# Kernel optimization log

Hardware: AMD Instinct MI355X
Metric: run time of the kernel (lower is better)

Reference implementation:

```python
import jax, jax.numpy as jnp
import numpy as np

V, E, H = 32000, 50, 100
B, T = 8, 512


def setup_inputs() -> dict:
    key = jax.random.key(0)
    ks = jax.random.split(key, 12)
    inputs = jax.random.randint(ks[0], (B, T), 0, V, dtype=jnp.int64)
    d = {
        "inputs": inputs,
        "embedding": jax.random.normal(ks[1], (V, E), jnp.float32),
        "W_hr": jax.random.normal(ks[2], (H, H), jnp.float32) * 0.01,
        "W_xr": jax.random.normal(ks[3], (E, H), jnp.float32) * 0.01,
        "b_r": jnp.zeros((H,), jnp.float32),
        "W_hz": jax.random.normal(ks[4], (H, H), jnp.float32) * 0.01,
        "W_xz": jax.random.normal(ks[5], (E, H), jnp.float32) * 0.01,
        "b_z": jnp.zeros((H,), jnp.float32),
        "W_hh": jax.random.normal(ks[6], (H, H), jnp.float32) * 0.01,
        "W_xh": jax.random.normal(ks[7], (E, H), jnp.float32) * 0.01,
        "b_h": jnp.zeros((H,), jnp.float32),
        "fc_W": jax.random.normal(ks[8], (H, V), jnp.float32) * 0.01,
        "fc_b": jnp.zeros((V,), jnp.float32),
    }
    return d


def reference(inputs, embedding, W_hr, W_xr, b_r, W_hz, W_xz, b_z,
              W_hh, W_xh, b_h, fc_W, fc_b):
    # Embed all timesteps at once: [B, T, E] -> time-major [T, B, E]
    x = embedding[inputs]
    x_tm = jnp.transpose(x, (1, 0, 2))

    h0 = jnp.zeros((inputs.shape[0], W_hr.shape[0]), dtype=embedding.dtype)

    def step(h_t, x_t):
        R_t = jax.nn.sigmoid(h_t @ W_hr + x_t @ W_xr + b_r)
        Z_t = jax.nn.sigmoid(h_t @ W_hz + x_t @ W_xz + b_z)
        # NOTE: original torch code computes (R_t * h_t) @ W_hh (left-to-right precedence)
        h_tilda = jnp.tanh((R_t * h_t) @ W_hh + x_t @ W_xh + b_h)
        h_new = Z_t * h_tilda + (1.0 - Z_t) * h_t
        y_t = h_new @ fc_W + fc_b  # [B, V]
        return h_new, y_t

    _, ys = jax.lax.scan(step, h0, x_tm)  # ys: [T, B, V]
    return jnp.transpose(ys, (1, 0, 2))   # [B, T, V]
```

## Files before the change

kernel.cpp:

```cpp
#include <hip/hip_runtime.h>
#include <hip/hip_bf16.h>
#include <hip/hip_fp16.h>
#include <math.h>

#define NV 32000
#define NE 50
#define NH 100
#define NB 8
#define NT 512
#define KP 112
#define HS 136

typedef __attribute__((ext_vector_type(8)))  _Float16 f16x8;
typedef __attribute__((ext_vector_type(4)))  float    f32x4;
typedef __attribute__((ext_vector_type(16))) float    f32x16;

__device__ __forceinline__ void bar_lgkm() {
    __builtin_amdgcn_sched_barrier(0);
    asm volatile("s_waitcnt lgkmcnt(0)" ::: "memory");
    __builtin_amdgcn_s_barrier();
    asm volatile("" ::: "memory");
    __builtin_amdgcn_sched_barrier(0);
}

__global__ __launch_bounds__(256) void convw_kernel(
    const float* __restrict__ W, _Float16* __restrict__ Wp)
{
    int wv = threadIdx.x >> 6, l = threadIdx.x & 63;
    int ct = blockIdx.x * 4 + wv;
    int v  = ct * 32 + (l & 31);
    int kb = (l >> 5) * 8;
    _Float16* dst = Wp + (size_t)ct * 7 * 512 + l * 8;
    for (int kt = 0; kt < 7; kt++) {
        f16x8 tmp;
        #pragma unroll
        for (int j = 0; j < 8; j++) {
            int k = kt * 16 + kb + j;
            tmp[j] = (_Float16)(k < NH ? W[(size_t)k * NV + v] : 0.0f);
        }
        *(f16x8*)(dst + (size_t)kt * 512) = tmp;
    }
}

__global__ __launch_bounds__(64) void convg_kernel(
    const float* __restrict__ Whr, const float* __restrict__ Whz,
    const float* __restrict__ Whh, _Float16* __restrict__ Wg)
{
    int f = blockIdx.x;
    int g = f / 28, rem = f % 28, n = rem / 4, kt = rem % 4;
    const float* W = (g == 0) ? Whr : (g == 1) ? Whz : Whh;
    int l   = threadIdx.x;
    int col = n * 16 + (l & 15);
    int k0  = kt * 32 + (l >> 4) * 8;
    f16x8 v;
    #pragma unroll
    for (int j = 0; j < 8; j++) {
        int k = k0 + j;
        v[j] = (_Float16)((k < NH && col < NH) ? W[k * NH + col] : 0.0f);
    }
    *(f16x8*)(Wg + (size_t)f * 512 + l * 8) = v;
}

__global__ __launch_bounds__(128) void xproj_kernel(
    const int* __restrict__ inp, const float* __restrict__ emb,
    const float* __restrict__ Wxr, const float* __restrict__ br,
    const float* __restrict__ Wxz, const float* __restrict__ bz,
    const float* __restrict__ Wxh, const float* __restrict__ bh,
    float* __restrict__ Xr, float* __restrict__ Xz, float* __restrict__ Xh)
{
    int n = blockIdx.x;
    int t = n >> 3, b = n & 7;
    __shared__ float xs[NE];
    int tid = threadIdx.x;
    int idx = inp[b * NT + t];
    if (tid < NE) xs[tid] = emb[idx * NE + tid];
    __syncthreads();
    if (tid < NH) {
        float ar = br[tid], az = bz[tid], ah = bh[tid];
        for (int e = 0; e < NE; e++) {
            float x = xs[e];
            ar += x * Wxr[e * NH + tid];
            az += x * Wxz[e * NH + tid];
            ah += x * Wxh[e * NH + tid];
        }
        Xr[n * NH + tid] = ar;
        Xz[n * NH + tid] = az;
        Xh[n * NH + tid] = ah;
    }
}

__global__ __launch_bounds__(256) void gru_rec_kernel(
    const _Float16* __restrict__ Wg,
    const float* __restrict__ Xr, const float* __restrict__ Xz,
    const float* __restrict__ Xh, _Float16* __restrict__ Hp)
{
    int b   = blockIdx.x;
    int tid = threadIdx.x;
    int w   = tid >> 6, l = tid & 63;
    int lj  = l & 15;

    __shared__ __align__(16) _Float16 h16[16 * HS];
    __shared__ __align__(16) _Float16 rh16[16 * HS];
    for (int i = tid; i < 16 * HS; i += 256) { h16[i] = (_Float16)0.0f; rh16[i] = (_Float16)0.0f; }
    __syncthreads();

    int n0 = w, n1 = w + 4;
    bool has1 = (n1 < 7);
    int n1c = has1 ? n1 : n0;

    f16x8 WR0[4], WZ0[4], WH0[4], WR1[4], WZ1[4], WH1[4];
    #pragma unroll
    for (int kt = 0; kt < 4; kt++) {
        WR0[kt] = *(const f16x8*)(Wg + (size_t)(((0*7 + n0)*4 + kt))*512 + l*8);
        WZ0[kt] = *(const f16x8*)(Wg + (size_t)(((1*7 + n0)*4 + kt))*512 + l*8);
        WH0[kt] = *(const f16x8*)(Wg + (size_t)(((2*7 + n0)*4 + kt))*512 + l*8);
        WR1[kt] = *(const f16x8*)(Wg + (size_t)(((0*7 + n1c)*4 + kt))*512 + l*8);
        WZ1[kt] = *(const f16x8*)(Wg + (size_t)(((1*7 + n1c)*4 + kt))*512 + l*8);
        WH1[kt] = *(const f16x8*)(Wg + (size_t)(((2*7 + n1c)*4 + kt))*512 + l*8);
    }

    int j0 = n0 * 16 + lj;
    int j1 = n1c * 16 + lj;
    int j0x = j0 < NH ? j0 : NH - 1;
    int j1x = j1 < NH ? j1 : NH - 1;

    float h0 = 0.0f, h1 = 0.0f;
    float xr0, xz0, xh0, xr1, xz1, xh1;
    if (l < 16) {
        int base = b * NH;
        xr0 = Xr[base + j0x]; xz0 = Xz[base + j0x]; xh0 = Xh[base + j0x];
        xr1 = Xr[base + j1x]; xz1 = Xz[base + j1x]; xh1 = Xh[base + j1x];
    }

    int aoff = lj * HS + (l >> 4) * 8;

    for (int t = 0; t < NT; t++) {
        float pr0, pz0, ph0, pr1, pz1, ph1;
        if (l < 16 && t + 1 < NT) {
            int base = ((t + 1) * NB + b) * NH;
            pr0 = Xr[base + j0x]; pz0 = Xz[base + j0x]; ph0 = Xh[base + j0x];
            pr1 = Xr[base + j1x]; pz1 = Xz[base + j1x]; ph1 = Xh[base + j1x];
        }

        f32x4 aR0 = {0,0,0,0}, aZ0 = {0,0,0,0}, aR1 = {0,0,0,0}, aZ1 = {0,0,0,0};
        #pragma unroll
        for (int kt = 0; kt < 4; kt++) {
            f16x8 a = *(const f16x8*)&h16[aoff + kt * 32];
            aR0 = __builtin_amdgcn_mfma_f32_16x16x32_f16(a, WR0[kt], aR0, 0, 0, 0);
            aZ0 = __builtin_amdgcn_mfma_f32_16x16x32_f16(a, WZ0[kt], aZ0, 0, 0, 0);
            aR1 = __builtin_amdgcn_mfma_f32_16x16x32_f16(a, WR1[kt], aR1, 0, 0, 0);
            aZ1 = __builtin_amdgcn_mfma_f32_16x16x32_f16(a, WZ1[kt], aZ1, 0, 0, 0);
        }
        float z0 = 0.0f, z1 = 0.0f;
        if (l < 16) {
            float r0 = 1.0f / (1.0f + __expf(-(aR0[0] + xr0)));
            z0       = 1.0f / (1.0f + __expf(-(aZ0[0] + xz0)));
            rh16[j0] = (_Float16)(j0 < NH ? r0 * h0 : 0.0f);
            if (has1) {
                float r1 = 1.0f / (1.0f + __expf(-(aR1[0] + xr1)));
                z1       = 1.0f / (1.0f + __expf(-(aZ1[0] + xz1)));
                rh16[j1] = (_Float16)(j1 < NH ? r1 * h1 : 0.0f);
            }
        }
        bar_lgkm();

        f32x4 aH0 = {0,0,0,0}, aH1 = {0,0,0,0};
        #pragma unroll
        for (int kt = 0; kt < 4; kt++) {
            f16x8 a = *(const f16x8*)&rh16[aoff + kt * 32];
            aH0 = __builtin_amdgcn_mfma_f32_16x16x32_f16(a, WH0[kt], aH0, 0, 0, 0);
            aH1 = __builtin_amdgcn_mfma_f32_16x16x32_f16(a, WH1[kt], aH1, 0, 0, 0);
        }
        if (l < 16) {
            size_t hpb = (size_t)(t * NB + b) * KP;
            {
                float e  = __expf(2.0f * (aH0[0] + xh0));
                float ht = 1.0f - 2.0f / (e + 1.0f);
                float hn = fmaf(z0, ht - h0, h0);
                hn = (j0 < NH) ? hn : 0.0f;
                h0 = hn;
                h16[j0] = (_Float16)hn;
                Hp[hpb + j0] = (_Float16)hn;
            }
            if (has1) {
                float e  = __expf(2.0f * (aH1[0] + xh1));
                float ht = 1.0f - 2.0f / (e + 1.0f);
                float hn = fmaf(z1, ht - h1, h1);
                hn = (j1 < NH) ? hn : 0.0f;
                h1 = hn;
                h16[j1] = (_Float16)hn;
                Hp[hpb + j1] = (_Float16)hn;
            }
        }
        bar_lgkm();

        xr0 = pr0; xz0 = pz0; xh0 = ph0;
        xr1 = pr1; xz1 = pz1; xh1 = ph1;
    }
}

__global__ __launch_bounds__(256) void outgemm_kernel(
    const _Float16* __restrict__ Hp, const _Float16* __restrict__ Wp,
    const float* __restrict__ fcb, float* __restrict__ out)
{
    int tid = threadIdx.x;
    int wv = tid >> 6, l = tid & 63;
    int n0 = blockIdx.x * 32;
    int cb = blockIdx.y * 256 + wv * 64;

    const _Float16* arow = Hp + (size_t)(n0 + (l & 31)) * KP + (l >> 5) * 8;
    f16x8 a[7];
    #pragma unroll
    for (int kt = 0; kt < 7; kt++)
        a[kt] = *(const f16x8*)(arow + kt * 16);

    int ct0 = cb >> 5;
    const _Float16* bp = Wp + (size_t)ct0 * 7 * 512 + l * 8;

    f32x16 acc0 = {0,0,0,0,0,0,0,0,0,0,0,0,0,0,0,0};
    f32x16 acc1 = {0,0,0,0,0,0,0,0,0,0,0,0,0,0,0,0};
    #pragma unroll
    for (int kt = 0; kt < 7; kt++) {
        f16x8 b0 = *(const f16x8*)(bp + (size_t)kt * 512);
        f16x8 b1 = *(const f16x8*)(bp + (size_t)(kt + 7) * 512);
        acc0 = __builtin_amdgcn_mfma_f32_32x32x16_f16(a[kt], b0, acc0, 0, 0, 0);
        acc1 = __builtin_amdgcn_mfma_f32_32x32x16_f16(a[kt], b1, acc1, 0, 0, 0);
    }

    int c0 = cb + (l & 31);
    float bias0 = fcb[c0], bias1 = fcb[c0 + 32];
    #pragma unroll
    for (int p = 0; p < 16; p++) {
        int r = (p & 3) + 8 * (p >> 2) + 4 * (l >> 5);
        int m = n0 + r;
        size_t row = (size_t)(m & 7) * NT + (m >> 3);
        out[row * NV + c0]      = acc0[p] + bias0;
        out[row * NV + c0 + 32] = acc1[p] + bias1;
    }
}

extern "C" void kernel_launch(void* const* d_in, const int* in_sizes, int n_in,
                              void* d_out, int out_size, void* d_ws, size_t ws_size,
                              hipStream_t stream)
{
    const int*   inp = (const int*)  d_in[0];
    const float* emb = (const float*)d_in[1];
    const float* Whr = (const float*)d_in[2];
    const float* Wxr = (const float*)d_in[3];
    const float* br  = (const float*)d_in[4];
    const float* Whz = (const float*)d_in[5];
    const float* Wxz = (const float*)d_in[6];
    const float* bz  = (const float*)d_in[7];
    const float* Whh = (const float*)d_in[8];
    const float* Wxh = (const float*)d_in[9];
    const float* bh  = (const float*)d_in[10];
    const float* fcW = (const float*)d_in[11];
    const float* fcb = (const float*)d_in[12];
    float* out = (float*)d_out;

    float*    Xr = (float*)d_ws;
    float*    Xz = Xr + NT * NB * NH;
    float*    Xh = Xz + NT * NB * NH;
    _Float16* Hp = (_Float16*)(Xh + NT * NB * NH);
    _Float16* Wp = Hp + (size_t)NT * NB * KP;
    _Float16* Wg = Wp + (size_t)1000 * 7 * 512;

    convw_kernel<<<NV / 32 / 4, 256, 0, stream>>>(fcW, Wp);
    convg_kernel<<<84, 64, 0, stream>>>(Whr, Whz, Whh, Wg);
    xproj_kernel<<<NT * NB, 128, 0, stream>>>(inp, emb, Wxr, br, Wxz, bz, Wxh, bh,
                                              Xr, Xz, Xh);
    gru_rec_kernel<<<NB, 256, 0, stream>>>(Wg, Xr, Xz, Xh, Hp);
    dim3 ggrid(NT * NB / 32, NV / 256);
    outgemm_kernel<<<ggrid, 256, 0, stream>>>(Hp, Wp, fcb, out);
}
```

Baseline: 636.8 us.

## Fuse GRU recurrence and output GEMM into a persistent producer-consumer kernel

```diff
diff --git a/kernel.cpp b/kernel.cpp
--- a/kernel.cpp
+++ b/kernel.cpp
@@ -11,6 +11,12 @@
 #define KP 112
 #define HS 136
 
+#define NBLK   256
+#define NCONS  (NBLK - NB)
+#define NMT    (NT * NB / 32)
+#define NNT    (NV / 256)
+#define NTILE  (NMT * NNT)
+
 typedef __attribute__((ext_vector_type(8)))  _Float16 f16x8;
 typedef __attribute__((ext_vector_type(4)))  float    f32x4;
 typedef __attribute__((ext_vector_type(16))) float    f32x16;
@@ -21,6 +27,11 @@
     __builtin_amdgcn_s_barrier();
     asm volatile("" ::: "memory");
     __builtin_amdgcn_sched_barrier(0);
+}
+
+__global__ void init_kernel(int* __restrict__ ctr)
+{
+    if (threadIdx.x < NB) ctr[threadIdx.x] = 0;
 }
 
 __global__ __launch_bounds__(256) void convw_kernel(
@@ -89,153 +100,183 @@
     }
 }
 
-__global__ __launch_bounds__(256) void gru_rec_kernel(
+__global__ __launch_bounds__(256) void fused_kernel(
     const _Float16* __restrict__ Wg,
     const float* __restrict__ Xr, const float* __restrict__ Xz,
-    const float* __restrict__ Xh, _Float16* __restrict__ Hp)
-{
-    int b   = blockIdx.x;
-    int tid = threadIdx.x;
-    int w   = tid >> 6, l = tid & 63;
-    int lj  = l & 15;
-
+    const float* __restrict__ Xh, _Float16* __restrict__ Hp,
+    const _Float16* __restrict__ Wp, const float* __restrict__ fcb,
+    float* __restrict__ out, int* __restrict__ ctr)
+{
     __shared__ __align__(16) _Float16 h16[16 * HS];
     __shared__ __align__(16) _Float16 rh16[16 * HS];
-    for (int i = tid; i < 16 * HS; i += 256) { h16[i] = (_Float16)0.0f; rh16[i] = (_Float16)0.0f; }
-    __syncthreads();
-
-    int n0 = w, n1 = w + 4;
-    bool has1 = (n1 < 7);
-    int n1c = has1 ? n1 : n0;
-
-    f16x8 WR0[4], WZ0[4], WH0[4], WR1[4], WZ1[4], WH1[4];
-    #pragma unroll
-    for (int kt = 0; kt < 4; kt++) {
-        WR0[kt] = *(const f16x8*)(Wg + (size_t)(((0*7 + n0)*4 + kt))*512 + l*8);
-        WZ0[kt] = *(const f16x8*)(Wg + (size_t)(((1*7 + n0)*4 + kt))*512 + l*8);
-        WH0[kt] = *(const f16x8*)(Wg + (size_t)(((2*7 + n0)*4 + kt))*512 + l*8);
-        WR1[kt] = *(const f16x8*)(Wg + (size_t)(((0*7 + n1c)*4 + kt))*512 + l*8);
-        WZ1[kt] = *(const f16x8*)(Wg + (size_t)(((1*7 + n1c)*4 + kt))*512 + l*8);
-        WH1[kt] = *(const f16x8*)(Wg + (size_t)(((2*7 + n1c)*4 + kt))*512 + l*8);
-    }
-
-    int j0 = n0 * 16 + lj;
-    int j1 = n1c * 16 + lj;
-    int j0x = j0 < NH ? j0 : NH - 1;
-    int j1x = j1 < NH ? j1 : NH - 1;
-
-    float h0 = 0.0f, h1 = 0.0f;
-    float xr0, xz0, xh0, xr1, xz1, xh1;
-    if (l < 16) {
-        int base = b * NH;
-        xr0 = Xr[base + j0x]; xz0 = Xz[base + j0x]; xh0 = Xh[base + j0x];
-        xr1 = Xr[base + j1x]; xz1 = Xz[base + j1x]; xh1 = Xh[base + j1x];
-    }
-
-    int aoff = lj * HS + (l >> 4) * 8;
-
-    for (int t = 0; t < NT; t++) {
-        float pr0, pz0, ph0, pr1, pz1, ph1;
-        if (l < 16 && t + 1 < NT) {
-            int base = ((t + 1) * NB + b) * NH;
-            pr0 = Xr[base + j0x]; pz0 = Xz[base + j0x]; ph0 = Xh[base + j0x];
-            pr1 = Xr[base + j1x]; pz1 = Xz[base + j1x]; ph1 = Xh[base + j1x];
-        }
-
-        f32x4 aR0 = {0,0,0,0}, aZ0 = {0,0,0,0}, aR1 = {0,0,0,0}, aZ1 = {0,0,0,0};
+
+    int tid = threadIdx.x;
+
+    if (blockIdx.x < NB) {
+        __builtin_amdgcn_s_setprio(1);
+        int b   = blockIdx.x;
+        int w   = tid >> 6, l = tid & 63;
+        int lj  = l & 15;
+
+        for (int i = tid; i < 16 * HS; i += 256) { h16[i] = (_Float16)0.0f; rh16[i] = (_Float16)0.0f; }
+        __syncthreads();
+
+        int n0 = w, n1 = w + 4;
+        bool has1 = (n1 < 7);
+        int n1c = has1 ? n1 : n0;
+
+        f16x8 WR0[4], WZ0[4], WH0[4], WR1[4], WZ1[4], WH1[4];
         #pragma unroll
         for (int kt = 0; kt < 4; kt++) {
-            f16x8 a = *(const f16x8*)&h16[aoff + kt * 32];
-            aR0 = __builtin_amdgcn_mfma_f32_16x16x32_f16(a, WR0[kt], aR0, 0, 0, 0);
-            aZ0 = __builtin_amdgcn_mfma_f32_16x16x32_f16(a, WZ0[kt], aZ0, 0, 0, 0);
-            aR1 = __builtin_amdgcn_mfma_f32_16x16x32_f16(a, WR1[kt], aR1, 0, 0, 0);
-            aZ1 = __builtin_amdgcn_mfma_f32_16x16x32_f16(a, WZ1[kt], aZ1, 0, 0, 0);
-        }
-        float z0 = 0.0f, z1 = 0.0f;
+            WR0[kt] = *(const f16x8*)(Wg + (size_t)(((0*7 + n0)*4 + kt))*512 + l*8);
+            WZ0[kt] = *(const f16x8*)(Wg + (size_t)(((1*7 + n0)*4 + kt))*512 + l*8);
+            WH0[kt] = *(const f16x8*)(Wg + (size_t)(((2*7 + n0)*4 + kt))*512 + l*8);
+            WR1[kt] = *(const f16x8*)(Wg + (size_t)(((0*7 + n1c)*4 + kt))*512 + l*8);
+            WZ1[kt] = *(const f16x8*)(Wg + (size_t)(((1*7 + n1c)*4 + kt))*512 + l*8);
+            WH1[kt] = *(const f16x8*)(Wg + (size_t)(((2*7 + n1c)*4 + kt))*512 + l*8);
+        }
+
+        int j0 = n0 * 16 + lj;
+        int j1 = n1c * 16 + lj;
+        int j0x = j0 < NH ? j0 : NH - 1;
+        int j1x = j1 < NH ? j1 : NH - 1;
+
+        float h0 = 0.0f, h1 = 0.0f;
+        float xr0, xz0, xh0, xr1, xz1, xh1;
         if (l < 16) {
-            float r0 = 1.0f / (1.0f + __expf(-(aR0[0] + xr0)));
-            z0       = 1.0f / (1.0f + __expf(-(aZ0[0] + xz0)));
-            rh16[j0] = (_Float16)(j0 < NH ? r0 * h0 : 0.0f);
-            if (has1) {
-                float r1 = 1.0f / (1.0f + __expf(-(aR1[0] + xr1)));
-                z1       = 1.0f / (1.0f + __expf(-(aZ1[0] + xz1)));
-                rh16[j1] = (_Float16)(j1 < NH ? r1 * h1 : 0.0f);
-            }
-        }
-        bar_lgkm();
-
-        f32x4 aH0 = {0,0,0,0}, aH1 = {0,0,0,0};
-        #pragma unroll
-        for (int kt = 0; kt < 4; kt++) {
-            f16x8 a = *(const f16x8*)&rh16[aoff + kt * 32];
-            aH0 = __builtin_amdgcn_mfma_f32_16x16x32_f16(a, WH0[kt], aH0, 0, 0, 0);
-            aH1 = __builtin_amdgcn_mfma_f32_16x16x32_f16(a, WH1[kt], aH1, 0, 0, 0);
-        }
-        if (l < 16) {
-            size_t hpb = (size_t)(t * NB + b) * KP;
-            {
-                float e  = __expf(2.0f * (aH0[0] + xh0));
-                float ht = 1.0f - 2.0f / (e + 1.0f);
-                float hn = fmaf(z0, ht - h0, h0);
-                hn = (j0 < NH) ? hn : 0.0f;
-                h0 = hn;
-                h16[j0] = (_Float16)hn;
-                Hp[hpb + j0] = (_Float16)hn;
-            }
-            if (has1) {
-                float e  = __expf(2.0f * (aH1[0] + xh1));
-                float ht = 1.0f - 2.0f / (e + 1.0f);
-                float hn = fmaf(z1, ht - h1, h1);
-                hn = (j1 < NH) ? hn : 0.0f;
-                h1 = hn;
-                h16[j1] = (_Float16)hn;
-                Hp[hpb + j1] = (_Float16)hn;
-            }
-        }
-        bar_lgkm();
-
-        xr0 = pr0; xz0 = pz0; xh0 = ph0;
-        xr1 = pr1; xz1 = pz1; xh1 = ph1;
-    }
-}
-
-__global__ __launch_bounds__(256) void outgemm_kernel(
-    const _Float16* __restrict__ Hp, const _Float16* __restrict__ Wp,
-    const float* __restrict__ fcb, float* __restrict__ out)
-{
-    int tid = threadIdx.x;
-    int wv = tid >> 6, l = tid & 63;
-    int n0 = blockIdx.x * 32;
-    int cb = blockIdx.y * 256 + wv * 64;
-
-    const _Float16* arow = Hp + (size_t)(n0 + (l & 31)) * KP + (l >> 5) * 8;
-    f16x8 a[7];
-    #pragma unroll
-    for (int kt = 0; kt < 7; kt++)
-        a[kt] = *(const f16x8*)(arow + kt * 16);
-
-    int ct0 = cb >> 5;
-    const _Float16* bp = Wp + (size_t)ct0 * 7 * 512 + l * 8;
-
-    f32x16 acc0 = {0,0,0,0,0,0,0,0,0,0,0,0,0,0,0,0};
-    f32x16 acc1 = {0,0,0,0,0,0,0,0,0,0,0,0,0,0,0,0};
-    #pragma unroll
-    for (int kt = 0; kt < 7; kt++) {
-        f16x8 b0 = *(const f16x8*)(bp + (size_t)kt * 512);
-        f16x8 b1 = *(const f16x8*)(bp + (size_t)(kt + 7) * 512);
-        acc0 = __builtin_amdgcn_mfma_f32_32x32x16_f16(a[kt], b0, acc0, 0, 0, 0);
-        acc1 = __builtin_amdgcn_mfma_f32_32x32x16_f16(a[kt], b1, acc1, 0, 0, 0);
-    }
-
-    int c0 = cb + (l & 31);
-    float bias0 = fcb[c0], bias1 = fcb[c0 + 32];
-    #pragma unroll
-    for (int p = 0; p < 16; p++) {
-        int r = (p & 3) + 8 * (p >> 2) + 4 * (l >> 5);
-        int m = n0 + r;
-        size_t row = (size_t)(m & 7) * NT + (m >> 3);
-        out[row * NV + c0]      = acc0[p] + bias0;
-        out[row * NV + c0 + 32] = acc1[p] + bias1;
+            int base = b * NH;
+            xr0 = Xr[base + j0x]; xz0 = Xz[base + j0x]; xh0 = Xh[base + j0x];
+            xr1 = Xr[base + j1x]; xz1 = Xz[base + j1x]; xh1 = Xh[base + j1x];
+        }
+
+        int aoff = lj * HS + (l >> 4) * 8;
+
+        for (int t = 0; t < NT; t++) {
+            float pr0, pz0, ph0, pr1, pz1, ph1;
+            if (l < 16 && t + 1 < NT) {
+                int base = ((t + 1) * NB + b) * NH;
+                pr0 = Xr[base + j0x]; pz0 = Xz[base + j0x]; ph0 = Xh[base + j0x];
+                pr1 = Xr[base + j1x]; pz1 = Xz[base + j1x]; ph1 = Xh[base + j1x];
+            }
+
+            f32x4 aR0 = {0,0,0,0}, aZ0 = {0,0,0,0}, aR1 = {0,0,0,0}, aZ1 = {0,0,0,0};
+            #pragma unroll
+            for (int kt = 0; kt < 4; kt++) {
+                f16x8 a = *(const f16x8*)&h16[aoff + kt * 32];
+                aR0 = __builtin_amdgcn_mfma_f32_16x16x32_f16(a, WR0[kt], aR0, 0, 0, 0);
+                aZ0 = __builtin_amdgcn_mfma_f32_16x16x32_f16(a, WZ0[kt], aZ0, 0, 0, 0);
+                aR1 = __builtin_amdgcn_mfma_f32_16x16x32_f16(a, WR1[kt], aR1, 0, 0, 0);
+                aZ1 = __builtin_amdgcn_mfma_f32_16x16x32_f16(a, WZ1[kt], aZ1, 0, 0, 0);
+            }
+            float z0 = 0.0f, z1 = 0.0f;
+            if (l < 16) {
+                float r0 = 1.0f / (1.0f + __expf(-(aR0[0] + xr0)));
+                z0       = 1.0f / (1.0f + __expf(-(aZ0[0] + xz0)));
+                rh16[j0] = (_Float16)(j0 < NH ? r0 * h0 : 0.0f);
+                if (has1) {
+                    float r1 = 1.0f / (1.0f + __expf(-(aR1[0] + xr1)));
+                    z1       = 1.0f / (1.0f + __expf(-(aZ1[0] + xz1)));
+                    rh16[j1] = (_Float16)(j1 < NH ? r1 * h1 : 0.0f);
+                }
+            }
+            bar_lgkm();
+
+            f32x4 aH0 = {0,0,0,0}, aH1 = {0,0,0,0};
+            #pragma unroll
+            for (int kt = 0; kt < 4; kt++) {
+                f16x8 a = *(const f16x8*)&rh16[aoff + kt * 32];
+                aH0 = __builtin_amdgcn_mfma_f32_16x16x32_f16(a, WH0[kt], aH0, 0, 0, 0);
+                aH1 = __builtin_amdgcn_mfma_f32_16x16x32_f16(a, WH1[kt], aH1, 0, 0, 0);
+            }
+            if (l < 16) {
+                size_t hpb = (size_t)(t * NB + b) * KP;
+                {
+                    float e  = __expf(2.0f * (aH0[0] + xh0));
+                    float ht = 1.0f - 2.0f / (e + 1.0f);
+                    float hn = fmaf(z0, ht - h0, h0);
+                    hn = (j0 < NH) ? hn : 0.0f;
+                    h0 = hn;
+                    h16[j0] = (_Float16)hn;
+                    Hp[hpb + j0] = (_Float16)hn;
+                }
+                if (has1) {
+                    float e  = __expf(2.0f * (aH1[0] + xh1));
+                    float ht = 1.0f - 2.0f / (e + 1.0f);
+                    float hn = fmaf(z1, ht - h1, h1);
+                    hn = (j1 < NH) ? hn : 0.0f;
+                    h1 = hn;
+                    h16[j1] = (_Float16)hn;
+                    Hp[hpb + j1] = (_Float16)hn;
+                }
+            }
+            bar_lgkm();
+
+            if ((t & 7) == 7) {
+                asm volatile("s_waitcnt vmcnt(0)" ::: "memory");
+                __syncthreads();
+                if (tid == 0)
+                    __hip_atomic_store(ctr + b, t + 1, __ATOMIC_RELEASE,
+                                       __HIP_MEMORY_SCOPE_AGENT);
+            }
+
+            xr0 = pr0; xz0 = pz0; xh0 = ph0;
+            xr1 = pr1; xz1 = pz1; xh1 = ph1;
+        }
+    } else {
+        int wv = tid >> 6, l = tid & 63;
+        int done_upto = 0;
+
+        for (int tile = (int)blockIdx.x - NB; tile < NTILE; tile += NCONS) {
+            int mt  = tile / NNT;
+            int ntl = tile - mt * NNT;
+            int need = mt * 4 + 4;
+
+            if (need > done_upto) {
+                if (tid == 0) {
+                    #pragma unroll 1
+                    for (int bi = 0; bi < NB; ++bi)
+                        while (__hip_atomic_load(ctr + bi, __ATOMIC_RELAXED,
+                                                 __HIP_MEMORY_SCOPE_AGENT) < need)
+                            __builtin_amdgcn_s_sleep(8);
+                }
+                __syncthreads();
+                __builtin_amdgcn_fence(__ATOMIC_ACQUIRE, "agent");
+                done_upto = need;
+            }
+
+            int n0 = mt * 32;
+            int cb = ntl * 256 + wv * 64;
+
+            const _Float16* arow = Hp + (size_t)(n0 + (l & 31)) * KP + (l >> 5) * 8;
+            f16x8 a[7];
+            #pragma unroll
+            for (int kt = 0; kt < 7; kt++)
+                a[kt] = *(const f16x8*)(arow + kt * 16);
+
+            int ct0 = cb >> 5;
+            const _Float16* bp = Wp + (size_t)ct0 * 7 * 512 + l * 8;
+
+            f32x16 acc0 = {0,0,0,0,0,0,0,0,0,0,0,0,0,0,0,0};
+            f32x16 acc1 = {0,0,0,0,0,0,0,0,0,0,0,0,0,0,0,0};
+            #pragma unroll
+            for (int kt = 0; kt < 7; kt++) {
+                f16x8 b0 = *(const f16x8*)(bp + (size_t)kt * 512);
+                f16x8 b1 = *(const f16x8*)(bp + (size_t)(kt + 7) * 512);
+                acc0 = __builtin_amdgcn_mfma_f32_32x32x16_f16(a[kt], b0, acc0, 0, 0, 0);
+                acc1 = __builtin_amdgcn_mfma_f32_32x32x16_f16(a[kt], b1, acc1, 0, 0, 0);
+            }
+
+            int c0 = cb + (l & 31);
+            float bias0 = fcb[c0], bias1 = fcb[c0 + 32];
+            #pragma unroll
+            for (int p = 0; p < 16; p++) {
+                int r = (p & 3) + 8 * (p >> 2) + 4 * (l >> 5);
+                int m = n0 + r;
+                size_t row = (size_t)(m & 7) * NT + (m >> 3);
+                out[row * NV + c0]      = acc0[p] + bias0;
+                out[row * NV + c0 + 32] = acc1[p] + bias1;
+            }
+        }
     }
 }
 
@@ -264,12 +305,12 @@
     _Float16* Hp = (_Float16*)(Xh + NT * NB * NH);
     _Float16* Wp = Hp + (size_t)NT * NB * KP;
     _Float16* Wg = Wp + (size_t)1000 * 7 * 512;
-
+    int*      ct = (int*)(Wg + (size_t)84 * 512);
+
+    init_kernel<<<1, 64, 0, stream>>>(ct);
     convw_kernel<<<NV / 32 / 4, 256, 0, stream>>>(fcW, Wp);
     convg_kernel<<<84, 64, 0, stream>>>(Whr, Whz, Whh, Wg);
     xproj_kernel<<<NT * NB, 128, 0, stream>>>(inp, emb, Wxr, br, Wxz, bz, Wxh, bh,
                                               Xr, Xz, Xh);
-    gru_rec_kernel<<<NB, 256, 0, stream>>>(Wg, Xr, Xz, Xh, Hp);
-    dim3 ggrid(NT * NB / 32, NV / 256);
-    outgemm_kernel<<<ggrid, 256, 0, stream>>>(Hp, Wp, fcb, out);
-}
+    fused_kernel<<<NBLK, 256, 0, stream>>>(Wg, Xr, Xz, Xh, Hp, Wp, fcb, out, ct);
+}
```

Measured after the change: 962.9 us. +51.2%, slower.

## Run GRU recurrence in a single wavefront per batch with register-resident weights

Applied to the files above, without the earlier changes.

```diff
diff --git a/kernel.cpp b/kernel.cpp
--- a/kernel.cpp
+++ b/kernel.cpp
@@ -9,19 +9,10 @@
 #define NB 8
 #define NT 512
 #define KP 112
-#define HS 136
 
 typedef __attribute__((ext_vector_type(8)))  _Float16 f16x8;
 typedef __attribute__((ext_vector_type(4)))  float    f32x4;
 typedef __attribute__((ext_vector_type(16))) float    f32x16;
-
-__device__ __forceinline__ void bar_lgkm() {
-    __builtin_amdgcn_sched_barrier(0);
-    asm volatile("s_waitcnt lgkmcnt(0)" ::: "memory");
-    __builtin_amdgcn_s_barrier();
-    asm volatile("" ::: "memory");
-    __builtin_amdgcn_sched_barrier(0);
-}
 
 __global__ __launch_bounds__(256) void convw_kernel(
     const float* __restrict__ W, _Float16* __restrict__ Wp)
@@ -89,113 +80,118 @@
     }
 }
 
-__global__ __launch_bounds__(256) void gru_rec_kernel(
+__global__ __launch_bounds__(64, 1) void gru_rec_kernel(
     const _Float16* __restrict__ Wg,
     const float* __restrict__ Xr, const float* __restrict__ Xz,
     const float* __restrict__ Xh, _Float16* __restrict__ Hp)
 {
-    int b   = blockIdx.x;
-    int tid = threadIdx.x;
-    int w   = tid >> 6, l = tid & 63;
-    int lj  = l & 15;
-
-    __shared__ __align__(16) _Float16 h16[16 * HS];
-    __shared__ __align__(16) _Float16 rh16[16 * HS];
-    for (int i = tid; i < 16 * HS; i += 256) { h16[i] = (_Float16)0.0f; rh16[i] = (_Float16)0.0f; }
+    const int b  = blockIdx.x;
+    const int l  = threadIdx.x;
+    const int kg = l >> 4;
+
+    __shared__ __align__(16) _Float16 h16[128];
+    __shared__ __align__(16) _Float16 rh16[128];
+    h16[l]  = (_Float16)0.0f;  h16[l + 64]  = (_Float16)0.0f;
+    rh16[l] = (_Float16)0.0f;  rh16[l + 64] = (_Float16)0.0f;
     __syncthreads();
 
-    int n0 = w, n1 = w + 4;
-    bool has1 = (n1 < 7);
-    int n1c = has1 ? n1 : n0;
-
-    f16x8 WR0[4], WZ0[4], WH0[4], WR1[4], WZ1[4], WH1[4];
-    #pragma unroll
-    for (int kt = 0; kt < 4; kt++) {
-        WR0[kt] = *(const f16x8*)(Wg + (size_t)(((0*7 + n0)*4 + kt))*512 + l*8);
-        WZ0[kt] = *(const f16x8*)(Wg + (size_t)(((1*7 + n0)*4 + kt))*512 + l*8);
-        WH0[kt] = *(const f16x8*)(Wg + (size_t)(((2*7 + n0)*4 + kt))*512 + l*8);
-        WR1[kt] = *(const f16x8*)(Wg + (size_t)(((0*7 + n1c)*4 + kt))*512 + l*8);
-        WZ1[kt] = *(const f16x8*)(Wg + (size_t)(((1*7 + n1c)*4 + kt))*512 + l*8);
-        WH1[kt] = *(const f16x8*)(Wg + (size_t)(((2*7 + n1c)*4 + kt))*512 + l*8);
-    }
-
-    int j0 = n0 * 16 + lj;
-    int j1 = n1c * 16 + lj;
-    int j0x = j0 < NH ? j0 : NH - 1;
-    int j1x = j1 < NH ? j1 : NH - 1;
-
-    float h0 = 0.0f, h1 = 0.0f;
-    float xr0, xz0, xh0, xr1, xz1, xh1;
+    f16x8 WB[3][7][4];
+    #pragma unroll
+    for (int g = 0; g < 3; g++)
+        #pragma unroll
+        for (int n = 0; n < 7; n++)
+            #pragma unroll
+            for (int kt = 0; kt < 4; kt++)
+                WB[g][n][kt] = *(const f16x8*)(Wg + (size_t)((g*7 + n)*4 + kt)*512 + l*8);
+
+    float hcol[7], zv[7], xcr[7], xcz[7], xch[7];
+    int   cx[7];
+    #pragma unroll
+    for (int n = 0; n < 7; n++) {
+        hcol[n] = 0.f; zv[n] = 0.f; xcr[n] = 0.f; xcz[n] = 0.f; xch[n] = 0.f;
+        int c = n * 16 + l;
+        cx[n] = c < NH ? c : NH - 1;
+    }
+
     if (l < 16) {
         int base = b * NH;
-        xr0 = Xr[base + j0x]; xz0 = Xz[base + j0x]; xh0 = Xh[base + j0x];
-        xr1 = Xr[base + j1x]; xz1 = Xz[base + j1x]; xh1 = Xh[base + j1x];
-    }
-
-    int aoff = lj * HS + (l >> 4) * 8;
+        #pragma unroll
+        for (int n = 0; n < 7; n++) {
+            xcr[n] = Xr[base + cx[n]];
+            xcz[n] = Xz[base + cx[n]];
+            xch[n] = Xh[base + cx[n]];
+        }
+    }
 
     for (int t = 0; t < NT; t++) {
-        float pr0, pz0, ph0, pr1, pz1, ph1;
+        f16x8 Ah[4];
+        #pragma unroll
+        for (int kt = 0; kt < 4; kt++)
+            Ah[kt] = *(const f16x8*)&h16[kg * 8 + kt * 32];
+
+        f32x4 aR[7], aZ[7];
+        #pragma unroll
+        for (int n = 0; n < 7; n++) {
+            aR[n] = (f32x4){xcr[n], 0.f, 0.f, 0.f};
+            aZ[n] = (f32x4){xcz[n], 0.f, 0.f, 0.f};
+        }
         if (l < 16 && t + 1 < NT) {
             int base = ((t + 1) * NB + b) * NH;
-            pr0 = Xr[base + j0x]; pz0 = Xz[base + j0x]; ph0 = Xh[base + j0x];
-            pr1 = Xr[base + j1x]; pz1 = Xz[base + j1x]; ph1 = Xh[base + j1x];
-        }
-
-        f32x4 aR0 = {0,0,0,0}, aZ0 = {0,0,0,0}, aR1 = {0,0,0,0}, aZ1 = {0,0,0,0};
+            #pragma unroll
+            for (int n = 0; n < 7; n++) {
+                xcr[n] = Xr[base + cx[n]];
+                xcz[n] = Xz[base + cx[n]];
+            }
+        }
         #pragma unroll
         for (int kt = 0; kt < 4; kt++) {
-            f16x8 a = *(const f16x8*)&h16[aoff + kt * 32];
-            aR0 = __builtin_amdgcn_mfma_f32_16x16x32_f16(a, WR0[kt], aR0, 0, 0, 0);
-            aZ0 = __builtin_amdgcn_mfma_f32_16x16x32_f16(a, WZ0[kt], aZ0, 0, 0, 0);
-            aR1 = __builtin_amdgcn_mfma_f32_16x16x32_f16(a, WR1[kt], aR1, 0, 0, 0);
-            aZ1 = __builtin_amdgcn_mfma_f32_16x16x32_f16(a, WZ1[kt], aZ1, 0, 0, 0);
-        }
-        float z0 = 0.0f, z1 = 0.0f;
+            #pragma unroll
+            for (int n = 0; n < 7; n++) {
+                aR[n] = __builtin_amdgcn_mfma_f32_16x16x32_f16(Ah[kt], WB[0][n][kt], aR[n], 0, 0, 0);
+                aZ[n] = __builtin_amdgcn_mfma_f32_16x16x32_f16(Ah[kt], WB[1][n][kt], aZ[n], 0, 0, 0);
+            }
+        }
         if (l < 16) {
-            float r0 = 1.0f / (1.0f + __expf(-(aR0[0] + xr0)));
-            z0       = 1.0f / (1.0f + __expf(-(aZ0[0] + xz0)));
-            rh16[j0] = (_Float16)(j0 < NH ? r0 * h0 : 0.0f);
-            if (has1) {
-                float r1 = 1.0f / (1.0f + __expf(-(aR1[0] + xr1)));
-                z1       = 1.0f / (1.0f + __expf(-(aZ1[0] + xz1)));
-                rh16[j1] = (_Float16)(j1 < NH ? r1 * h1 : 0.0f);
-            }
-        }
-        bar_lgkm();
-
-        f32x4 aH0 = {0,0,0,0}, aH1 = {0,0,0,0};
-        #pragma unroll
-        for (int kt = 0; kt < 4; kt++) {
-            f16x8 a = *(const f16x8*)&rh16[aoff + kt * 32];
-            aH0 = __builtin_amdgcn_mfma_f32_16x16x32_f16(a, WH0[kt], aH0, 0, 0, 0);
-            aH1 = __builtin_amdgcn_mfma_f32_16x16x32_f16(a, WH1[kt], aH1, 0, 0, 0);
-        }
+            #pragma unroll
+            for (int n = 0; n < 7; n++) {
+                float r = 1.0f / (1.0f + __expf(-aR[n][0]));
+                zv[n]   = 1.0f / (1.0f + __expf(-aZ[n][0]));
+                rh16[n * 16 + l] = (_Float16)(r * hcol[n]);
+            }
+        }
+
+        f16x8 Ar[4];
+        #pragma unroll
+        for (int kt = 0; kt < 4; kt++)
+            Ar[kt] = *(const f16x8*)&rh16[kg * 8 + kt * 32];
+
+        f32x4 aH[7];
+        #pragma unroll
+        for (int n = 0; n < 7; n++) aH[n] = (f32x4){xch[n], 0.f, 0.f, 0.f};
+        if (l < 16 && t + 1 < NT) {
+            int base = ((t + 1) * NB + b) * NH;
+            #pragma unroll
+            for (int n = 0; n < 7; n++) xch[n] = Xh[base + cx[n]];
+        }
+        #pragma unroll
+        for (int kt = 0; kt < 4; kt++)
+            #pragma unroll
+            for (int n = 0; n < 7; n++)
+                aH[n] = __builtin_amdgcn_mfma_f32_16x16x32_f16(Ar[kt], WB[2][n][kt], aH[n], 0, 0, 0);
+
         if (l < 16) {
-            size_t hpb = (size_t)(t * NB + b) * KP;
-            {
-                float e  = __expf(2.0f * (aH0[0] + xh0));
-                float ht = 1.0f - 2.0f / (e + 1.0f);
-                float hn = fmaf(z0, ht - h0, h0);
-                hn = (j0 < NH) ? hn : 0.0f;
-                h0 = hn;
-                h16[j0] = (_Float16)hn;
-                Hp[hpb + j0] = (_Float16)hn;
-            }
-            if (has1) {
-                float e  = __expf(2.0f * (aH1[0] + xh1));
-                float ht = 1.0f - 2.0f / (e + 1.0f);
-                float hn = fmaf(z1, ht - h1, h1);
-                hn = (j1 < NH) ? hn : 0.0f;
-                h1 = hn;
-                h16[j1] = (_Float16)hn;
-                Hp[hpb + j1] = (_Float16)hn;
-            }
-        }
-        bar_lgkm();
-
-        xr0 = pr0; xz0 = pz0; xh0 = ph0;
-        xr1 = pr1; xz1 = pz1; xh1 = ph1;
+            size_t hb = (size_t)(t * NB + b) * KP;
+            #pragma unroll
+            for (int n = 0; n < 7; n++) {
+                float e  = __expf(2.0f * (aH[n][0]));
+                float th = 1.0f - 2.0f / (e + 1.0f);
+                float hn = fmaf(zv[n], th - hcol[n], hcol[n]);
+                hn = (n * 16 + l < NH) ? hn : 0.0f;
+                hcol[n] = hn;
+                h16[n * 16 + l] = (_Float16)hn;
+                Hp[hb + n * 16 + l] = (_Float16)hn;
+            }
+        }
     }
 }
 
@@ -269,7 +265,7 @@
     convg_kernel<<<84, 64, 0, stream>>>(Whr, Whz, Whh, Wg);
     xproj_kernel<<<NT * NB, 128, 0, stream>>>(inp, emb, Wxr, br, Wxz, bz, Wxh, bh,
                                               Xr, Xz, Xh);
-    gru_rec_kernel<<<NB, 256, 0, stream>>>(Wg, Xr, Xz, Xh, Hp);
+    gru_rec_kernel<<<NB, 64, 0, stream>>>(Wg, Xr, Xz, Xh, Hp);
     dim3 ggrid(NT * NB / 32, NV / 256);
     outgemm_kernel<<<ggrid, 256, 0, stream>>>(Hp, Wp, fcb, out);
 }
```

Result: slower. 1.390 ms (+118.3%).
